# Kernel optimization log

Measured on AMD Instinct MI355X. Metric: run time of the kernel, lower is better.

Reference implementation:

```python
import jax, jax.numpy as jnp
import numpy as np

B, Q, K, H = 16, 512, 512, 64
DQ, DK, DV = 256, 256, 256
MASK_VAL = -1000000.0


def setup_inputs() -> dict:
    key = jax.random.key(0)
    ks = jax.random.split(key, 7)
    queries = jax.random.normal(ks[0], (B, Q, DQ), dtype=jnp.float32)
    keys = jax.random.normal(ks[1], (B, K, DK), dtype=jnp.float32)
    values = jax.random.normal(ks[2], (B, K, DV), dtype=jnp.float32)
    valid_lens = jax.random.randint(ks[3], (B,), 1, K + 1).astype(jnp.int32)
    # learned params (nn.Linear, bias=False): weight shape [out, in]
    Wq = jax.random.normal(ks[4], (H, DQ), dtype=jnp.float32) / np.sqrt(DQ)
    Wk = jax.random.normal(ks[5], (H, DK), dtype=jnp.float32) / np.sqrt(DK)
    wv = jax.random.normal(ks[6], (H,), dtype=jnp.float32) / np.sqrt(H)
    return {"queries": queries, "keys": keys, "values": values,
            "valid_lens": valid_lens, "Wq": Wq, "Wk": Wk, "wv": wv}


def reference(queries, keys, values, valid_lens, Wq, Wk, wv):
    q = jnp.einsum('bqd,hd->bqh', queries, Wq)          # [B,Q,H]
    k = jnp.einsum('bkd,hd->bkh', keys, Wk)             # [B,K,H]
    feats = jnp.tanh(q[:, :, None, :] + k[:, None, :, :])  # [B,Q,K,H]
    scores = jnp.einsum('bqkh,h->bqk', feats, wv)       # [B,Q,K]
    kmask = jnp.arange(K)[None, None, :] < valid_lens[:, None, None]
    scores = jnp.where(kmask, scores, MASK_VAL)
    attn = jax.nn.softmax(scores, axis=-1)              # [B,Q,K]
    return jnp.einsum('bqk,bkv->bqv', attn, values)     # [B,Q,DV]
```

## Files before the change

kernel.cpp:

```cpp
#include <hip/hip_runtime.h>
#include <math.h>

#if defined(__has_builtin)
#  if __has_builtin(__builtin_amdgcn_exp2f)
#    define EXP2F(x) __builtin_amdgcn_exp2f(x)
#  endif
#  if __has_builtin(__builtin_amdgcn_rcpf)
#    define RCPF(x) __builtin_amdgcn_rcpf(x)
#  endif
#endif
#ifndef EXP2F
#  define EXP2F(x) exp2f(x)
#endif
#ifndef RCPF
#  define RCPF(x) (1.0f/(x))
#endif

static constexpr int Bn = 16, QN = 512, KN = 512, Hn = 64, DV = 256, DIN = 256;
static constexpr int TQ = 4;
static constexpr float TWO_LOG2E = 2.8853900817779268f;
static constexpr float LOG2E     = 1.4426950408889634f;

typedef __attribute__((ext_vector_type(8))) short short8;
typedef __attribute__((ext_vector_type(4))) float f32x4;

__device__ __forceinline__ short f2bf(float x) {
  unsigned u = __builtin_bit_cast(unsigned, x);
  u += 0x7FFF + ((u >> 16) & 1);
  return (short)(u >> 16);
}
__device__ __forceinline__ float bf2f(short h) {
  return __builtin_bit_cast(float, ((unsigned)(unsigned short)h) << 16);
}

__global__ __launch_bounds__(256) void proj_mfma(
    const float* __restrict__ queries, const float* __restrict__ keys,
    const float* __restrict__ Wq, const float* __restrict__ Wk,
    const float* __restrict__ wv,
    float* __restrict__ qT, float* __restrict__ ekT, float* __restrict__ wv2)
{
  __shared__ float tr[4][16][20];
  int t = threadIdx.x;
  int lane = t & 63, wid = t >> 6;
  if (blockIdx.x == 0 && t < Hn) wv2[t] = 2.0f * wv[t];
  bool is_k = blockIdx.x >= 512;
  int trow = (blockIdx.x & 511) * 16;
  const float* X = is_k ? keys : queries;
  const float* W = is_k ? Wk : Wq;
  float* dT = is_k ? ekT : qT;
  int mr = lane & 15, quad = lane >> 4;
  const float* xp = X + (size_t)(trow + mr) * DIN + quad * 8;
  const float* wp = W + (size_t)(wid * 16 + mr) * DIN + quad * 8;

  f32x4 acc = (f32x4){0.f, 0.f, 0.f, 0.f};
  #pragma unroll
  for (int kc = 0; kc < 8; ++kc) {
    float4 a0 = *(const float4*)(xp + kc * 32);
    float4 a1 = *(const float4*)(xp + kc * 32 + 4);
    float4 b0 = *(const float4*)(wp + kc * 32);
    float4 b1 = *(const float4*)(wp + kc * 32 + 4);
    float av[8] = {a0.x, a0.y, a0.z, a0.w, a1.x, a1.y, a1.z, a1.w};
    float bv[8] = {b0.x, b0.y, b0.z, b0.w, b1.x, b1.y, b1.z, b1.w};
    short8 ah, al, bh, bl;
    #pragma unroll
    for (int j = 0; j < 8; ++j) {
      ah[j] = f2bf(av[j]);
      al[j] = f2bf(av[j] - bf2f(ah[j]));
      bh[j] = f2bf(bv[j]);
      bl[j] = f2bf(bv[j] - bf2f(bh[j]));
    }
    acc = __builtin_amdgcn_mfma_f32_16x16x32_bf16(al, bh, acc, 0, 0, 0);
    acc = __builtin_amdgcn_mfma_f32_16x16x32_bf16(ah, bl, acc, 0, 0, 0);
    acc = __builtin_amdgcn_mfma_f32_16x16x32_bf16(ah, bh, acc, 0, 0, 0);
  }
  #pragma unroll
  for (int reg = 0; reg < 4; ++reg)
    tr[wid][mr][quad * 4 + reg] = EXP2F(acc[reg] * TWO_LOG2E);
  int b = trow >> 9, rr = trow & 511;
  #pragma unroll
  for (int hp = 0; hp < 4; ++hp) {
    int h_l = hp * 4 + quad, r_l = mr;
    dT[((size_t)b * Hn + wid * 16 + h_l) * 512 + rr + r_l] = tr[wid][h_l][r_l];
  }
}

__global__ __launch_bounds__(512) void attn_kernel(
    const float* __restrict__ qT,
    const float* __restrict__ ekT,
    const float* __restrict__ values,
    const int*   __restrict__ valid_lens,
    const float* __restrict__ wv2,
    float* __restrict__ out)
{
  __shared__ __align__(16) float pt[KN][TQ];
  __shared__ __align__(16) float pacc[TQ][DV];
  __shared__ float wsum[8][TQ];
  __shared__ float inv_s[TQ];
  __shared__ int srank[Bn];

  int t = threadIdx.x;
  int lane = t & 63, wave = t >> 6;

  if (t < Bn) {
    int Lb = valid_lens[t];
    int r = 0;
    #pragma unroll
    for (int b2 = 0; b2 < Bn; ++b2) {
      int L2 = valid_lens[b2];
      r += (L2 > Lb || (L2 == Lb && b2 < t)) ? 1 : 0;
    }
    srank[r] = t;
  }
  __syncthreads();

  int rank = blockIdx.x >> 7;
  int b = __builtin_amdgcn_readfirstlane(srank[rank]);
  int L = __builtin_amdgcn_readfirstlane(valid_lens[b]);
  int q0 = (blockIdx.x & 127) * TQ;

  float S = 0.f;
  #pragma unroll
  for (int h = 0; h < Hn; ++h) S += wv2[h];
  S *= 0.5f;

  {
    int k = t;
    float p[TQ];
    if (k < L) {
      float sc[TQ];
      #pragma unroll
      for (int r = 0; r < TQ; ++r) sc[r] = S;
      const float* kb = ekT + (size_t)b * Hn * KN + k;
      const float* qb = qT  + (size_t)b * Hn * QN + q0;
      for (int h0 = 0; h0 < Hn; h0 += 8) {
        float ekv[8];
        #pragma unroll
        for (int j = 0; j < 8; ++j)
          ekv[j] = kb[(size_t)(h0 + j) * KN];
        #pragma unroll
        for (int jp = 0; jp < 4; ++jp) {
          int ha = h0 + 2 * jp;
          float wa = wv2[ha], wb = wv2[ha + 1];
          float4 qa = *(const float4*)(qb + (size_t)ha * QN);
          float4 qc = *(const float4*)(qb + (size_t)(ha + 1) * QN);
          float eka = ekv[2 * jp], ekb = ekv[2 * jp + 1];
          float da, db, num;
          da = qa.x * eka + 1.0f; db = qc.x * ekb + 1.0f;
          num = wa * db + wb * da; sc[0] -= num * RCPF(da * db);
          da = qa.y * eka + 1.0f; db = qc.y * ekb + 1.0f;
          num = wa * db + wb * da; sc[1] -= num * RCPF(da * db);
          da = qa.z * eka + 1.0f; db = qc.z * ekb + 1.0f;
          num = wa * db + wb * da; sc[2] -= num * RCPF(da * db);
          da = qa.w * eka + 1.0f; db = qc.w * ekb + 1.0f;
          num = wa * db + wb * da; sc[3] -= num * RCPF(da * db);
        }
      }
      #pragma unroll
      for (int r = 0; r < TQ; ++r) p[r] = EXP2F(sc[r] * LOG2E);
      *(float4*)&pt[k][0] = make_float4(p[0], p[1], p[2], p[3]);
    } else {
      #pragma unroll
      for (int r = 0; r < TQ; ++r) p[r] = 0.f;
    }
    #pragma unroll
    for (int r = 0; r < TQ; ++r) {
      float s = p[r];
      #pragma unroll
      for (int off = 32; off > 0; off >>= 1) s += __shfl_xor(s, off, 64);
      if (lane == r) wsum[wave][r] = s;
    }
  }
  __syncthreads();
  if (t < TQ) {
    float s = 0.f;
    #pragma unroll
    for (int w = 0; w < 8; ++w) s += wsum[w][t];
    inv_s[t] = 1.0f / s;
  }

  int c = t & (DV - 1), half = t >> 8;
  int mid = L >> 1;
  int k0 = half ? mid : 0;
  int k1 = half ? L : mid;
  float acc[TQ] = {0.f, 0.f, 0.f, 0.f};
  const float* vb = values + (size_t)b * KN * DV + c;
  #pragma unroll 4
  for (int k = k0; k < k1; ++k) {
    float val = vb[(size_t)k * DV];
    float4 pa = *(const float4*)&pt[k][0];
    acc[0] += pa.x * val; acc[1] += pa.y * val;
    acc[2] += pa.z * val; acc[3] += pa.w * val;
  }
  if (half) {
    #pragma unroll
    for (int r = 0; r < TQ; ++r) pacc[r][c] = acc[r];
  }
  __syncthreads();
  if (!half) {
    float* ob = out + (size_t)(b * QN + q0) * DV + c;
    #pragma unroll
    for (int r = 0; r < TQ; ++r)
      ob[(size_t)r * DV] = (acc[r] + pacc[r][c]) * inv_s[r];
  }
}

extern "C" void kernel_launch(void* const* d_in, const int* in_sizes, int n_in,
                              void* d_out, int out_size, void* d_ws, size_t ws_size,
                              hipStream_t stream) {
  const float* queries    = (const float*)d_in[0];
  const float* keys       = (const float*)d_in[1];
  const float* values     = (const float*)d_in[2];
  const int*   valid_lens = (const int*)d_in[3];
  const float* Wq         = (const float*)d_in[4];
  const float* Wk         = (const float*)d_in[5];
  const float* wv         = (const float*)d_in[6];
  float* out = (float*)d_out;

  char* ws = (char*)d_ws;
  float* qT  = (float*)ws;
  float* ekT = qT + (size_t)Bn * Hn * QN;
  float* wv2 = ekT + (size_t)Bn * Hn * KN;

  proj_mfma<<<1024, 256, 0, stream>>>(queries, keys, Wq, Wk, wv, qT, ekT, wv2);
  attn_kernel<<<Bn * (QN / TQ), 512, 0, stream>>>(qT, ekT, values,
                                                  valid_lens, wv2, out);
}
```

Measured before the change: 143.9 us.

## Split PV over eight key ranges per wave with float4 columns, prefetch key features

The attention-times-values stage is restructured. Previously two halves of the block each handled one column per thread; now each of the eight waves takes one eighth of the valid key range and each lane computes four columns with float4 value loads. Partial sums from seven waves go through a larger shared buffer and wave 0 reduces them and writes float4 outputs. The score loop also fully unrolls over heads and prefetches the next eight key-feature values, trading extra registers and shared memory for fewer, wider global loads and more memory-level parallelism.

```diff
diff --git a/kernel.cpp b/kernel.cpp
--- a/kernel.cpp
+++ b/kernel.cpp
@@ -18,6 +18,7 @@
 
 static constexpr int Bn = 16, QN = 512, KN = 512, Hn = 64, DV = 256, DIN = 256;
 static constexpr int TQ = 4;
+static constexpr int NSPLIT = 8;
 static constexpr float TWO_LOG2E = 2.8853900817779268f;
 static constexpr float LOG2E     = 1.4426950408889634f;
 
@@ -32,6 +33,11 @@
 __device__ __forceinline__ float bf2f(short h) {
   return __builtin_bit_cast(float, ((unsigned)(unsigned short)h) << 16);
 }
+#define FMA4(a, s, v) \
+  { (a).x += (s) * (v).x; (a).y += (s) * (v).y; \
+    (a).z += (s) * (v).z; (a).w += (s) * (v).w; }
+#define ADD4(a, v) \
+  { (a).x += (v).x; (a).y += (v).y; (a).z += (v).z; (a).w += (v).w; }
 
 __global__ __launch_bounds__(256) void proj_mfma(
     const float* __restrict__ queries, const float* __restrict__ keys,
@@ -93,7 +99,7 @@
     float* __restrict__ out)
 {
   __shared__ __align__(16) float pt[KN][TQ];
-  __shared__ __align__(16) float pacc[TQ][DV];
+  __shared__ __align__(16) float pacc[NSPLIT - 1][TQ][DV];
   __shared__ float wsum[8][TQ];
   __shared__ float inv_s[TQ];
   __shared__ int srank[Bn];
@@ -130,13 +136,20 @@
       float sc[TQ];
       #pragma unroll
       for (int r = 0; r < TQ; ++r) sc[r] = S;
-      const float* kb = ekT + (size_t)b * Hn * KN + k;
+      const float* kp = ekT + (size_t)b * Hn * KN + k;
       const float* qb = qT  + (size_t)b * Hn * QN + q0;
+      float ekv[8];
+      #pragma unroll
+      for (int j = 0; j < 8; ++j)
+        ekv[j] = kp[(size_t)j * KN];
+      #pragma unroll
       for (int h0 = 0; h0 < Hn; h0 += 8) {
-        float ekv[8];
-        #pragma unroll
-        for (int j = 0; j < 8; ++j)
-          ekv[j] = kb[(size_t)(h0 + j) * KN];
+        float ekn[8];
+        if (h0 + 8 < Hn) {
+          #pragma unroll
+          for (int j = 0; j < 8; ++j)
+            ekn[j] = kp[(size_t)(h0 + 8 + j) * KN];
+        }
         #pragma unroll
         for (int jp = 0; jp < 4; ++jp) {
           int ha = h0 + 2 * jp;
@@ -154,6 +167,10 @@
           da = qa.w * eka + 1.0f; db = qc.w * ekb + 1.0f;
           num = wa * db + wb * da; sc[3] -= num * RCPF(da * db);
         }
+        if (h0 + 8 < Hn) {
+          #pragma unroll
+          for (int j = 0; j < 8; ++j) ekv[j] = ekn[j];
+        }
       }
       #pragma unroll
       for (int r = 0; r < TQ; ++r) p[r] = EXP2F(sc[r] * LOG2E);
@@ -178,29 +195,55 @@
     inv_s[t] = 1.0f / s;
   }
 
-  int c = t & (DV - 1), half = t >> 8;
-  int mid = L >> 1;
-  int k0 = half ? mid : 0;
-  int k1 = half ? L : mid;
-  float acc[TQ] = {0.f, 0.f, 0.f, 0.f};
-  const float* vb = values + (size_t)b * KN * DV + c;
-  #pragma unroll 4
-  for (int k = k0; k < k1; ++k) {
-    float val = vb[(size_t)k * DV];
-    float4 pa = *(const float4*)&pt[k][0];
-    acc[0] += pa.x * val; acc[1] += pa.y * val;
-    acc[2] += pa.z * val; acc[3] += pa.w * val;
-  }
-  if (half) {
-    #pragma unroll
-    for (int r = 0; r < TQ; ++r) pacc[r][c] = acc[r];
+  int g = wave;
+  int c4 = lane * 4;
+  int klo = (L * g) >> 3, khi = (L * (g + 1)) >> 3;
+  float4 a0 = {0.f,0.f,0.f,0.f}, a1 = a0, a2 = a0, a3 = a0;
+  const float* vb = values + (size_t)b * KN * DV + c4;
+  int k = klo;
+  #pragma unroll 2
+  for (; k + 2 <= khi; k += 2) {
+    float4 v0 = *(const float4*)(vb + (size_t)k * DV);
+    float4 v1 = *(const float4*)(vb + (size_t)(k + 1) * DV);
+    float4 p0 = *(const float4*)&pt[k][0];
+    float4 p1 = *(const float4*)&pt[k + 1][0];
+    FMA4(a0, p0.x, v0); FMA4(a1, p0.y, v0);
+    FMA4(a2, p0.z, v0); FMA4(a3, p0.w, v0);
+    FMA4(a0, p1.x, v1); FMA4(a1, p1.y, v1);
+    FMA4(a2, p1.z, v1); FMA4(a3, p1.w, v1);
+  }
+  if (k < khi) {
+    float4 v0 = *(const float4*)(vb + (size_t)k * DV);
+    float4 p0 = *(const float4*)&pt[k][0];
+    FMA4(a0, p0.x, v0); FMA4(a1, p0.y, v0);
+    FMA4(a2, p0.z, v0); FMA4(a3, p0.w, v0);
+  }
+  if (g > 0) {
+    *(float4*)&pacc[g - 1][0][c4] = a0;
+    *(float4*)&pacc[g - 1][1][c4] = a1;
+    *(float4*)&pacc[g - 1][2][c4] = a2;
+    *(float4*)&pacc[g - 1][3][c4] = a3;
   }
   __syncthreads();
-  if (!half) {
-    float* ob = out + (size_t)(b * QN + q0) * DV + c;
-    #pragma unroll
-    for (int r = 0; r < TQ; ++r)
-      ob[(size_t)r * DV] = (acc[r] + pacc[r][c]) * inv_s[r];
+  if (g == 0) {
+    #pragma unroll
+    for (int gg = 0; gg < NSPLIT - 1; ++gg) {
+      float4 x0 = *(const float4*)&pacc[gg][0][c4];
+      float4 x1 = *(const float4*)&pacc[gg][1][c4];
+      float4 x2 = *(const float4*)&pacc[gg][2][c4];
+      float4 x3 = *(const float4*)&pacc[gg][3][c4];
+      ADD4(a0, x0); ADD4(a1, x1); ADD4(a2, x2); ADD4(a3, x3);
+    }
+    float* ob = out + (size_t)(b * QN + q0) * DV + c4;
+    float i0 = inv_s[0], i1 = inv_s[1], i2 = inv_s[2], i3 = inv_s[3];
+    *(float4*)(ob + 0 * (size_t)DV) =
+        make_float4(a0.x * i0, a0.y * i0, a0.z * i0, a0.w * i0);
+    *(float4*)(ob + 1 * (size_t)DV) =
+        make_float4(a1.x * i1, a1.y * i1, a1.z * i1, a1.w * i1);
+    *(float4*)(ob + 2 * (size_t)DV) =
+        make_float4(a2.x * i2, a2.y * i2, a2.z * i2, a2.w * i2);
+    *(float4*)(ob + 3 * (size_t)DV) =
+        make_float4(a3.x * i3, a3.y * i3, a3.z * i3, a3.w * i3);
   }
 }
 
```

New measurement: 163.4 us. 13.5% more time.

## Warp-specialize attention kernel with double-buffered score/PV pipeline and balanced batch pairing

Applied to the files above, without the earlier changes.

Replaces the one-tile-per-block attention kernel with a persistent-style kernel of 512 blocks. In each block, four waves compute scores for the next 4-query tile into a double-buffered LDS array while the other four waves do the P·V product for the previous tile. Blocks are paired across long and short batches (rank m with 15-m) to balance work across CUs. The cost is that each wave group now handles the full key range serially with half as many threads per stage, and a block-wide barrier runs every step.

```diff
diff --git a/kernel.cpp b/kernel.cpp
--- a/kernel.cpp
+++ b/kernel.cpp
@@ -18,6 +18,7 @@
 
 static constexpr int Bn = 16, QN = 512, KN = 512, Hn = 64, DV = 256, DIN = 256;
 static constexpr int TQ = 4;
+static constexpr int NSTEP = 4;
 static constexpr float TWO_LOG2E = 2.8853900817779268f;
 static constexpr float LOG2E     = 1.4426950408889634f;
 
@@ -84,7 +85,7 @@
   }
 }
 
-__global__ __launch_bounds__(512) void attn_kernel(
+__global__ __launch_bounds__(512) void attn_ws(
     const float* __restrict__ qT,
     const float* __restrict__ ekT,
     const float* __restrict__ values,
@@ -92,10 +93,8 @@
     const float* __restrict__ wv2,
     float* __restrict__ out)
 {
-  __shared__ __align__(16) float pt[KN][TQ];
-  __shared__ __align__(16) float pacc[TQ][DV];
-  __shared__ float wsum[8][TQ];
-  __shared__ float inv_s[TQ];
+  __shared__ __align__(16) float pt[2][KN][TQ];
+  __shared__ float wsum[2][4][TQ];
   __shared__ int srank[Bn];
 
   int t = threadIdx.x;
@@ -113,94 +112,97 @@
   }
   __syncthreads();
 
-  int rank = blockIdx.x >> 7;
-  int b = __builtin_amdgcn_readfirstlane(srank[rank]);
+  int cu = blockIdx.x & 255, slot = blockIdx.x >> 8;
+  int m = cu >> 4;
+  int jr = slot ? 15 - m : m;
+  int b = __builtin_amdgcn_readfirstlane(srank[jr]);
   int L = __builtin_amdgcn_readfirstlane(valid_lens[b]);
-  int q0 = (blockIdx.x & 127) * TQ;
+  int qpart = (cu & 15) + (slot ? 16 : 0);
+  int qbase = qpart * (TQ * NSTEP);
 
   float S = 0.f;
   #pragma unroll
   for (int h = 0; h < Hn; ++h) S += wv2[h];
   S *= 0.5f;
 
-  {
-    int k = t;
-    float p[TQ];
-    if (k < L) {
-      float sc[TQ];
+  for (int g = 0; g <= NSTEP; ++g) {
+    if (wave < 4 && g < NSTEP) {
+      int buf = g & 1;
+      int q0 = qbase + g * TQ;
+      const float* qb = qT + (size_t)b * Hn * QN + q0;
+      float psum[TQ] = {0.f, 0.f, 0.f, 0.f};
       #pragma unroll
-      for (int r = 0; r < TQ; ++r) sc[r] = S;
-      const float* kb = ekT + (size_t)b * Hn * KN + k;
-      const float* qb = qT  + (size_t)b * Hn * QN + q0;
-      for (int h0 = 0; h0 < Hn; h0 += 8) {
-        float ekv[8];
+      for (int kk = 0; kk < 2; ++kk) {
+        int k = (t & 255) + kk * 256;
+        float p[TQ];
+        if (k < L) {
+          float sc[TQ];
+          #pragma unroll
+          for (int r = 0; r < TQ; ++r) sc[r] = S;
+          const float* kp = ekT + (size_t)b * Hn * KN + k;
+          for (int h0 = 0; h0 < Hn; h0 += 8) {
+            float ekv[8];
+            #pragma unroll
+            for (int j = 0; j < 8; ++j)
+              ekv[j] = kp[(size_t)(h0 + j) * KN];
+            #pragma unroll
+            for (int jp = 0; jp < 4; ++jp) {
+              int ha = h0 + 2 * jp;
+              float wa = wv2[ha], wb = wv2[ha + 1];
+              float4 qa = *(const float4*)(qb + (size_t)ha * QN);
+              float4 qc = *(const float4*)(qb + (size_t)(ha + 1) * QN);
+              float eka = ekv[2 * jp], ekb = ekv[2 * jp + 1];
+              float da, db, num;
+              da = qa.x * eka + 1.0f; db = qc.x * ekb + 1.0f;
+              num = wa * db + wb * da; sc[0] -= num * RCPF(da * db);
+              da = qa.y * eka + 1.0f; db = qc.y * ekb + 1.0f;
+              num = wa * db + wb * da; sc[1] -= num * RCPF(da * db);
+              da = qa.z * eka + 1.0f; db = qc.z * ekb + 1.0f;
+              num = wa * db + wb * da; sc[2] -= num * RCPF(da * db);
+              da = qa.w * eka + 1.0f; db = qc.w * ekb + 1.0f;
+              num = wa * db + wb * da; sc[3] -= num * RCPF(da * db);
+            }
+          }
+          #pragma unroll
+          for (int r = 0; r < TQ; ++r) p[r] = EXP2F(sc[r] * LOG2E);
+          *(float4*)&pt[buf][k][0] = make_float4(p[0], p[1], p[2], p[3]);
+        } else {
+          #pragma unroll
+          for (int r = 0; r < TQ; ++r) p[r] = 0.f;
+          *(float4*)&pt[buf][k][0] = make_float4(0.f, 0.f, 0.f, 0.f);
+        }
         #pragma unroll
-        for (int j = 0; j < 8; ++j)
-          ekv[j] = kb[(size_t)(h0 + j) * KN];
+        for (int r = 0; r < TQ; ++r) psum[r] += p[r];
+      }
+      #pragma unroll
+      for (int r = 0; r < TQ; ++r) {
+        float s = psum[r];
         #pragma unroll
-        for (int jp = 0; jp < 4; ++jp) {
-          int ha = h0 + 2 * jp;
-          float wa = wv2[ha], wb = wv2[ha + 1];
-          float4 qa = *(const float4*)(qb + (size_t)ha * QN);
-          float4 qc = *(const float4*)(qb + (size_t)(ha + 1) * QN);
-          float eka = ekv[2 * jp], ekb = ekv[2 * jp + 1];
-          float da, db, num;
-          da = qa.x * eka + 1.0f; db = qc.x * ekb + 1.0f;
-          num = wa * db + wb * da; sc[0] -= num * RCPF(da * db);
-          da = qa.y * eka + 1.0f; db = qc.y * ekb + 1.0f;
-          num = wa * db + wb * da; sc[1] -= num * RCPF(da * db);
-          da = qa.z * eka + 1.0f; db = qc.z * ekb + 1.0f;
-          num = wa * db + wb * da; sc[2] -= num * RCPF(da * db);
-          da = qa.w * eka + 1.0f; db = qc.w * ekb + 1.0f;
-          num = wa * db + wb * da; sc[3] -= num * RCPF(da * db);
-        }
-      }
+        for (int off = 32; off > 0; off >>= 1) s += __shfl_xor(s, off, 64);
+        if (lane == r) wsum[buf][wave][r] = s;
+      }
+    } else if (wave >= 4 && g > 0) {
+      int gg = g - 1, buf = gg & 1;
+      int q0 = qbase + gg * TQ;
+      int c = t - 256;
+      float acc[TQ] = {0.f, 0.f, 0.f, 0.f};
+      const float* vb = values + (size_t)b * KN * DV + c;
+      #pragma unroll 4
+      for (int k = 0; k < L; ++k) {
+        float val = vb[(size_t)k * DV];
+        float4 pa = *(const float4*)&pt[buf][k][0];
+        acc[0] += pa.x * val; acc[1] += pa.y * val;
+        acc[2] += pa.z * val; acc[3] += pa.w * val;
+      }
+      float* ob = out + (size_t)(b * QN + q0) * DV + c;
       #pragma unroll
-      for (int r = 0; r < TQ; ++r) p[r] = EXP2F(sc[r] * LOG2E);
-      *(float4*)&pt[k][0] = make_float4(p[0], p[1], p[2], p[3]);
-    } else {
-      #pragma unroll
-      for (int r = 0; r < TQ; ++r) p[r] = 0.f;
+      for (int r = 0; r < TQ; ++r) {
+        float s = wsum[buf][0][r] + wsum[buf][1][r]
+                + wsum[buf][2][r] + wsum[buf][3][r];
+        ob[(size_t)r * DV] = acc[r] * (1.0f / s);
+      }
     }
-    #pragma unroll
-    for (int r = 0; r < TQ; ++r) {
-      float s = p[r];
-      #pragma unroll
-      for (int off = 32; off > 0; off >>= 1) s += __shfl_xor(s, off, 64);
-      if (lane == r) wsum[wave][r] = s;
-    }
-  }
-  __syncthreads();
-  if (t < TQ) {
-    float s = 0.f;
-    #pragma unroll
-    for (int w = 0; w < 8; ++w) s += wsum[w][t];
-    inv_s[t] = 1.0f / s;
-  }
-
-  int c = t & (DV - 1), half = t >> 8;
-  int mid = L >> 1;
-  int k0 = half ? mid : 0;
-  int k1 = half ? L : mid;
-  float acc[TQ] = {0.f, 0.f, 0.f, 0.f};
-  const float* vb = values + (size_t)b * KN * DV + c;
-  #pragma unroll 4
-  for (int k = k0; k < k1; ++k) {
-    float val = vb[(size_t)k * DV];
-    float4 pa = *(const float4*)&pt[k][0];
-    acc[0] += pa.x * val; acc[1] += pa.y * val;
-    acc[2] += pa.z * val; acc[3] += pa.w * val;
-  }
-  if (half) {
-    #pragma unroll
-    for (int r = 0; r < TQ; ++r) pacc[r][c] = acc[r];
-  }
-  __syncthreads();
-  if (!half) {
-    float* ob = out + (size_t)(b * QN + q0) * DV + c;
-    #pragma unroll
-    for (int r = 0; r < TQ; ++r)
-      ob[(size_t)r * DV] = (acc[r] + pacc[r][c]) * inv_s[r];
+    __syncthreads();
   }
 }
 
@@ -222,6 +224,5 @@
   float* wv2 = ekT + (size_t)Bn * Hn * KN;
 
   proj_mfma<<<1024, 256, 0, stream>>>(queries, keys, Wq, Wk, wv, qT, ekT, wv2);
-  attn_kernel<<<Bn * (QN / TQ), 512, 0, stream>>>(qT, ekT, values,
-                                                  valid_lens, wv2, out);
-}
+  attn_ws<<<512, 512, 0, stream>>>(qT, ekT, values, valid_lens, wv2, out);
+}
```

Result: slower. 183.6 us (+27.6%).
